# Kernel tuning notes

Measured on AMD Instinct MI355X. Metric: run time of the kernel, lower is better.

The kernel has to match this reference:

```python
import jax, jax.numpy as jnp
import numpy as np

B, N, DK, DM = 8, 4096, 512, 64

def setup_inputs() -> dict:
    key = jax.random.key(0)
    ks = jax.random.split(key, 7)
    K = jax.random.normal(ks[0], (B, N, DK), dtype=jnp.float32)
    Q = jax.random.normal(ks[1], (B, N, DK), dtype=jnp.float32)
    V = jax.random.normal(ks[2], (B, N, DK), dtype=jnp.float32)
    s = 1.0 / np.sqrt(DK)
    Wk = jax.random.normal(ks[3], (DM, DK), dtype=jnp.float32) * s
    bk = jax.random.normal(ks[4], (DM,), dtype=jnp.float32) * 0.01
    Wq = jax.random.normal(ks[5], (DM, DK), dtype=jnp.float32) * s
    bq = jax.random.normal(ks[6], (DM,), dtype=jnp.float32) * 0.01
    return {"K": K, "Q": Q, "V": V, "Wk": Wk, "bk": bk, "Wq": Wq, "bq": bq}

def reference(K, Q, V, Wk, bk, Wq, bq):
    # Linear projections (torch Linear: x @ W.T + b)
    pk = jnp.einsum('bnd,md->bnm', K, Wk) + bk  # [B,N,DM]
    pq = jnp.einsum('bnd,md->bnm', Q, Wq) + bq  # [B,M,DM]
    scale = 1.0 / np.sqrt(DM).astype(np.float32)
    scores = jnp.einsum('bqm,bkm->bqk', pq, pk) * scale  # [B,M,N]
    attn = jax.nn.softmax(scores, axis=-1)
    return jnp.einsum('bqk,bkd->bqd', attn, V)  # V unprojected, as in original
```

## Files before the change

kernel.cpp:

```cpp
#include <hip/hip_runtime.h>
#include <hip/hip_bf16.h>
#include <cstdint>


#define DEVINL __device__ __forceinline__

using f32x4  = __attribute__((ext_vector_type(4)))  float;
using bf16x8 = __attribute__((ext_vector_type(8)))  short;
using bf16x4 = __attribute__((ext_vector_type(4)))  short;

constexpr int BATCH = 8;
constexpr int N     = 4096;
constexpr int DK    = 512;
constexpr int DM    = 64;
constexpr int KVB   = 64;
constexpr int QB    = 128;
constexpr int STEPS = N / KVB;

DEVINL short cvt_bf16(float x) {
  uint32_t u = __float_as_uint(x);
  uint32_t r = u + 0x7fffu + ((u >> 16) & 1u);
  return (short)(r >> 16);
}

DEVINL void async16(void* lds, const void* g) {
  __builtin_amdgcn_global_load_lds(
      (const __attribute__((address_space(1))) uint32_t*)(uintptr_t)g,
      (__attribute__((address_space(3))) uint32_t*)(uint32_t)(uintptr_t)lds,
      16, 0, 0);
}

DEVINL f32x4 mfma16(bf16x8 a, bf16x8 b, f32x4 c) {
  return __builtin_amdgcn_mfma_f32_16x16x32_bf16(a, b, c, 0, 0, 0);
}

__global__ __launch_bounds__(256) void wconv_kernel(
    const float* __restrict__ Wk, const float* __restrict__ Wq,
    short* __restrict__ WkB, short* __restrict__ WqB) {
  int i = blockIdx.x * 256 + threadIdx.x;
  WkB[i] = cvt_bf16(Wk[i]);
  WqB[i] = cvt_bf16(Wq[i]);
}

__global__ __launch_bounds__(256) void vtrans_kernel(
    const float* __restrict__ V, short* __restrict__ Vt) {
  int bb = blockIdx.x;
  int b  = bb >> 9;
  int nt = (bb >> 3) & 63;
  int dt = bb & 7;
  int n0 = nt * 64, d0 = dt * 64;
  __shared__ short t_lds[64][80];
  int tid = threadIdx.x;
#pragma unroll
  for (int it = 0; it < 4; ++it) {
    int idx = it * 256 + tid;
    int row = idx >> 4;
    int c4  = idx & 15;
    f32x4 v = *(const f32x4*)&V[((size_t)b * N + n0 + row) * DK + d0 + c4 * 4];
#pragma unroll
    for (int j = 0; j < 4; ++j) t_lds[c4 * 4 + j][row] = cvt_bf16(v[j]);
  }
  __syncthreads();
#pragma unroll
  for (int it = 0; it < 2; ++it) {
    int idx = it * 256 + tid;
    int rd = idx >> 3;
    int ck = idx & 7;
    bf16x8 vv = *(const bf16x8*)&t_lds[rd][ck * 8];
    *(bf16x8*)&Vt[((size_t)b * DK + d0 + rd) * N + n0 + ck * 8] = vv;
  }
}

__global__ __launch_bounds__(512, 2) void proj_kernel(
    const float* __restrict__ Q, const float* __restrict__ K,
    const short* __restrict__ WqB, const short* __restrict__ WkB,
    const float* __restrict__ bq, const float* __restrict__ bk,
    short* __restrict__ pq, short* __restrict__ pk) {
  bool isK = blockIdx.x >= 256;
  const float* X    = isK ? K : Q;
  const short* W    = isK ? WkB : WqB;
  const float* bias = isK ? bk : bq;
  short* P          = isK ? pk : pq;
  int rb = (blockIdx.x & 255) * 128;

  __shared__ short x_lds[128 * 512];
  int tid = threadIdx.x, w = tid >> 6, lane = tid & 63, g = lane >> 4, c = lane & 15;

#pragma unroll
  for (int it = 0; it < 32; ++it) {
    int idx4 = it * 512 + tid;
    int row  = idx4 >> 7;
    int col  = (idx4 & 127) * 4;
    f32x4 v = *(const f32x4*)&X[((size_t)rb + row) * DK + col];
    bf16x4 hb;
#pragma unroll
    for (int j = 0; j < 4; ++j) hb[j] = cvt_bf16(v[j]);
    int sc = (col >> 3) ^ (row & 7);
    *(bf16x4*)&x_lds[row * 512 + sc * 8 + ((col >> 2) & 1) * 4] = hb;
  }
  __syncthreads();

  f32x4 o[4];
#pragma unroll
  for (int mt = 0; mt < 4; ++mt) o[mt] = f32x4{0.f, 0.f, 0.f, 0.f};
  int arow = w * 16 + c;
#pragma unroll
  for (int ks = 0; ks < 16; ++ks) {
    int sc = (ks * 4 + g) ^ (arow & 7);
    bf16x8 a = *(const bf16x8*)&x_lds[arow * 512 + sc * 8];
#pragma unroll
    for (int mt = 0; mt < 4; ++mt) {
      bf16x8 bfr = *(const bf16x8*)&W[(size_t)(mt * 16 + c) * DK + ks * 32 + g * 8];
      o[mt] = mfma16(a, bfr, o[mt]);
    }
  }
#pragma unroll
  for (int mt = 0; mt < 4; ++mt) {
    float bb = bias[mt * 16 + c];
#pragma unroll
    for (int r = 0; r < 4; ++r) {
      int row = rb + w * 16 + g * 4 + r;
      P[(size_t)row * DM + mt * 16 + c] = cvt_bf16(o[mt][r] + bb);
    }
  }
}

__global__ __launch_bounds__(512, 2) void flash_kernel(
    const short* __restrict__ pq, const short* __restrict__ pk,
    const short* __restrict__ vt, float* __restrict__ out) {
  int b  = blockIdx.x & 7;
  int qt = blockIdx.x >> 3;
  int q0 = qt * QB;

  int tid = threadIdx.x, w = tid >> 6, lane = tid & 63, g = lane >> 4, c = lane & 15;

  __shared__ short pk_lds[KVB * DM];
  __shared__ short vt_lds[2][DK * KVB];
  __shared__ short p_lds[QB * KVB];
  __shared__ float alpha_lds[QB];
  __shared__ float lsum_lds[QB];

  const short* pk_b = pk + (size_t)b * N * DM;
  const short* vt_b = vt + (size_t)b * DK * N;

  const short* pq_row = pq + ((size_t)b * N + q0 + w * 16 + c) * DM;
  bf16x8 qf0 = *(const bf16x8*)(pq_row + g * 8);
  bf16x8 qf1 = *(const bf16x8*)(pq_row + 32 + g * 8);

  f32x4 acc[4][8];
#pragma unroll
  for (int i = 0; i < 4; ++i)
#pragma unroll
    for (int j = 0; j < 8; ++j) acc[i][j] = f32x4{0.f, 0.f, 0.f, 0.f};

  float m_run = -1e30f, l_run = 0.f;

  auto stage_pk = [&](int t) {
    int off16 = tid;
    int row = off16 >> 3, ck = off16 & 7;
    const short* src = pk_b + (size_t)(t * KVB + row) * DM + ((ck ^ (row & 7)) * 8);
    async16((void*)(pk_lds + (size_t)w * 512), (const void*)src);
  };
  auto stage_vt = [&](int t, int buf) {
#pragma unroll
    for (int r = 0; r < 8; ++r) {
      int off16 = r * 512 + tid;
      int row = off16 >> 3, ck = off16 & 7;
      const short* src = vt_b + (size_t)row * N + t * KVB + ((ck ^ (row & 7)) * 8);
      async16((void*)(&vt_lds[buf][0] + (size_t)(r * 512 + w * 64) * 8), (const void*)src);
    }
  };

  stage_pk(0);
  stage_vt(0, 0);
  __syncthreads();

  for (int t = 0; t < STEPS; ++t) {
    int buf = t & 1;
    if (t + 1 < STEPS) stage_vt(t + 1, buf ^ 1);

    float sv[16];
#pragma unroll
    for (int s = 0; s < 4; ++s) {
      int row = s * 16 + c;
      bf16x8 a0 = *(const bf16x8*)&pk_lds[row * 64 + ((g ^ (row & 7)) * 8)];
      bf16x8 a1 = *(const bf16x8*)&pk_lds[row * 64 + (((4 + g) ^ (row & 7)) * 8)];
      f32x4 d = f32x4{0.f, 0.f, 0.f, 0.f};
      d = mfma16(a0, qf0, d);
      d = mfma16(a1, qf1, d);
#pragma unroll
      for (int r = 0; r < 4; ++r) sv[s * 4 + r] = d[r] * 0.125f;
    }

    float tmax = sv[0];
#pragma unroll
    for (int j = 1; j < 16; ++j) tmax = fmaxf(tmax, sv[j]);
    tmax = fmaxf(tmax, __shfl_xor(tmax, 16));
    tmax = fmaxf(tmax, __shfl_xor(tmax, 32));
    float m_new = fmaxf(m_run, tmax);
    float alpha = __expf(m_run - m_new);
    float ts = 0.f;
#pragma unroll
    for (int j = 0; j < 16; ++j) { sv[j] = __expf(sv[j] - m_new); ts += sv[j]; }
    ts += __shfl_xor(ts, 16);
    ts += __shfl_xor(ts, 32);
    l_run = l_run * alpha + ts;
    m_run = m_new;

    int qrow = w * 16 + c;
    if (g == 0) alpha_lds[qrow] = alpha;
#pragma unroll
    for (int s = 0; s < 4; ++s) {
      bf16x4 pb;
#pragma unroll
      for (int r = 0; r < 4; ++r) pb[r] = cvt_bf16(sv[s * 4 + r]);
      int ck = (s * 2 + (g >> 1)) ^ (qrow & 7);
      *(bf16x4*)&p_lds[qrow * 64 + ck * 8 + (g & 1) * 4] = pb;
    }

    asm volatile("s_waitcnt lgkmcnt(0)" ::: "memory");
    __builtin_amdgcn_s_barrier();
    asm volatile("" ::: "memory");

    if (t + 1 < STEPS) stage_pk(t + 1);

    float al[8];
#pragma unroll
    for (int j = 0; j < 8; ++j) al[j] = alpha_lds[j * 16 + c];
#pragma unroll
    for (int i = 0; i < 4; ++i)
#pragma unroll
      for (int j = 0; j < 8; ++j) acc[i][j] *= al[j];

#pragma unroll
    for (int kh = 0; kh < 2; ++kh) {
      bf16x8 pf[8];
#pragma unroll
      for (int j = 0; j < 8; ++j) {
        int row = j * 16 + c;
        pf[j] = *(const bf16x8*)&p_lds[row * 64 + (((kh * 4 + g) ^ (row & 7)) * 8)];
      }
#pragma unroll
      for (int i = 0; i < 4; ++i) {
        int row = w * 64 + i * 16 + c;
        bf16x8 vf = *(const bf16x8*)&vt_lds[buf][row * 64 + (((kh * 4 + g) ^ (row & 7)) * 8)];
#pragma unroll
        for (int j = 0; j < 8; ++j) acc[i][j] = mfma16(vf, pf[j], acc[i][j]);
      }
    }
    __syncthreads();
  }

  if (g == 0) lsum_lds[w * 16 + c] = l_run;
  __syncthreads();

  float* out_b = out + (size_t)b * N * DK;
#pragma unroll
  for (int j = 0; j < 8; ++j) {
    float rl = 1.f / lsum_lds[j * 16 + c];
#pragma unroll
    for (int i = 0; i < 4; ++i)
#pragma unroll
      for (int r = 0; r < 4; ++r) {
        int q    = q0 + j * 16 + c;
        int vcol = w * 64 + i * 16 + g * 4 + r;
        out_b[(size_t)q * DK + vcol] = acc[i][j][r] * rl;
      }
  }
}

extern "C" void kernel_launch(void* const* d_in, const int* in_sizes, int n_in,
                              void* d_out, int out_size, void* d_ws, size_t ws_size,
                              hipStream_t stream) {
  (void)in_sizes; (void)n_in; (void)out_size; (void)ws_size;
  const float* K  = (const float*)d_in[0];
  const float* Q  = (const float*)d_in[1];
  const float* V  = (const float*)d_in[2];
  const float* Wk = (const float*)d_in[3];
  const float* bk = (const float*)d_in[4];
  const float* Wq = (const float*)d_in[5];
  const float* bq = (const float*)d_in[6];
  float* out = (float*)d_out;

  char* ws = (char*)d_ws;
  short* pq  = (short*)(ws + 0);
  short* pk  = (short*)(ws + ((size_t)4 << 20));
  short* vt  = (short*)(ws + ((size_t)8 << 20));
  short* WqB = (short*)(ws + ((size_t)40 << 20));
  short* WkB = (short*)(ws + ((size_t)40 << 20) + 64 * 512 * 2);

  hipLaunchKernelGGL(wconv_kernel,  dim3(128),  dim3(256), 0, stream, Wk, Wq, WkB, WqB);
  hipLaunchKernelGGL(vtrans_kernel, dim3(4096), dim3(256), 0, stream, V, vt);
  hipLaunchKernelGGL(proj_kernel,   dim3(512),  dim3(512), 0, stream, Q, K, WqB, WkB, bq, bk, pq, pk);
  hipLaunchKernelGGL(flash_kernel,  dim3(256),  dim3(512), 0, stream, pq, pk, vt, out);
}
```

Before: 267.5 us.

## Software-pipeline flash loop: overlap next QK softmax with PV MFMAs, lazy rescale

```diff
diff --git a/kernel.cpp b/kernel.cpp
--- a/kernel.cpp
+++ b/kernel.cpp
@@ -81,6 +81,7 @@
   const short* W    = isK ? WkB : WqB;
   const float* bias = isK ? bk : bq;
   short* P          = isK ? pk : pq;
+  float sc          = isK ? 1.0f : 0.125f;
   int rb = (blockIdx.x & 255) * 128;
 
   __shared__ short x_lds[128 * 512];
@@ -95,8 +96,8 @@
     bf16x4 hb;
 #pragma unroll
     for (int j = 0; j < 4; ++j) hb[j] = cvt_bf16(v[j]);
-    int sc = (col >> 3) ^ (row & 7);
-    *(bf16x4*)&x_lds[row * 512 + sc * 8 + ((col >> 2) & 1) * 4] = hb;
+    int scz = (col >> 3) ^ (row & 7);
+    *(bf16x4*)&x_lds[row * 512 + scz * 8 + ((col >> 2) & 1) * 4] = hb;
   }
   __syncthreads();
 
@@ -106,8 +107,8 @@
   int arow = w * 16 + c;
 #pragma unroll
   for (int ks = 0; ks < 16; ++ks) {
-    int sc = (ks * 4 + g) ^ (arow & 7);
-    bf16x8 a = *(const bf16x8*)&x_lds[arow * 512 + sc * 8];
+    int scz = (ks * 4 + g) ^ (arow & 7);
+    bf16x8 a = *(const bf16x8*)&x_lds[arow * 512 + scz * 8];
 #pragma unroll
     for (int mt = 0; mt < 4; ++mt) {
       bf16x8 bfr = *(const bf16x8*)&W[(size_t)(mt * 16 + c) * DK + ks * 32 + g * 8];
@@ -120,7 +121,7 @@
 #pragma unroll
     for (int r = 0; r < 4; ++r) {
       int row = rb + w * 16 + g * 4 + r;
-      P[(size_t)row * DM + mt * 16 + c] = cvt_bf16(o[mt][r] + bb);
+      P[(size_t)row * DM + mt * 16 + c] = cvt_bf16((o[mt][r] + bb) * sc);
     }
   }
 }
@@ -133,6 +134,7 @@
   int q0 = qt * QB;
 
   int tid = threadIdx.x, w = tid >> 6, lane = tid & 63, g = lane >> 4, c = lane & 15;
+  int qrow = w * 16 + c;
 
   __shared__ short pk_lds[KVB * DM];
   __shared__ short vt_lds[2][DK * KVB];
@@ -143,7 +145,7 @@
   const short* pk_b = pk + (size_t)b * N * DM;
   const short* vt_b = vt + (size_t)b * DK * N;
 
-  const short* pq_row = pq + ((size_t)b * N + q0 + w * 16 + c) * DM;
+  const short* pq_row = pq + ((size_t)b * N + q0 + qrow) * DM;
   bf16x8 qf0 = *(const bf16x8*)(pq_row + g * 8);
   bf16x8 qf1 = *(const bf16x8*)(pq_row + 32 + g * 8);
 
@@ -156,8 +158,7 @@
   float m_run = -1e30f, l_run = 0.f;
 
   auto stage_pk = [&](int t) {
-    int off16 = tid;
-    int row = off16 >> 3, ck = off16 & 7;
+    int row = tid >> 3, ck = tid & 7;
     const short* src = pk_b + (size_t)(t * KVB + row) * DM + ((ck ^ (row & 7)) * 8);
     async16((void*)(pk_lds + (size_t)w * 512), (const void*)src);
   };
@@ -175,11 +176,10 @@
   stage_vt(0, 0);
   __syncthreads();
 
-  for (int t = 0; t < STEPS; ++t) {
-    int buf = t & 1;
-    if (t + 1 < STEPS) stage_vt(t + 1, buf ^ 1);
-
-    float sv[16];
+  float sv[16];
+  bf16x4 pb[4];
+  float alpha;
+  {
 #pragma unroll
     for (int s = 0; s < 4; ++s) {
       int row = s * 16 + c;
@@ -189,49 +189,161 @@
       d = mfma16(a0, qf0, d);
       d = mfma16(a1, qf1, d);
 #pragma unroll
-      for (int r = 0; r < 4; ++r) sv[s * 4 + r] = d[r] * 0.125f;
-    }
-
+      for (int r = 0; r < 4; ++r) sv[s * 4 + r] = d[r];
+    }
     float tmax = sv[0];
 #pragma unroll
     for (int j = 1; j < 16; ++j) tmax = fmaxf(tmax, sv[j]);
     tmax = fmaxf(tmax, __shfl_xor(tmax, 16));
     tmax = fmaxf(tmax, __shfl_xor(tmax, 32));
-    float m_new = fmaxf(m_run, tmax);
-    float alpha = __expf(m_run - m_new);
+    m_run = tmax;
     float ts = 0.f;
 #pragma unroll
-    for (int j = 0; j < 16; ++j) { sv[j] = __expf(sv[j] - m_new); ts += sv[j]; }
+    for (int j = 0; j < 16; ++j) { sv[j] = __expf(sv[j] - m_run); ts += sv[j]; }
+    ts += __shfl_xor(ts, 16);
+    ts += __shfl_xor(ts, 32);
+    l_run = ts;
+    alpha = 1.0f;
+#pragma unroll
+    for (int s = 0; s < 4; ++s)
+#pragma unroll
+      for (int r = 0; r < 4; ++r) pb[s][r] = cvt_bf16(sv[s * 4 + r]);
+  }
+  asm volatile("s_waitcnt lgkmcnt(0)" ::: "memory");
+  __builtin_amdgcn_s_barrier();
+#pragma unroll
+  for (int s = 0; s < 4; ++s) {
+    int ck = (s * 2 + (g >> 1)) ^ (qrow & 7);
+    *(bf16x4*)&p_lds[qrow * 64 + ck * 8 + (g & 1) * 4] = pb[s];
+  }
+  if (g == 0) alpha_lds[qrow] = alpha;
+  stage_pk(1);
+  asm volatile("s_waitcnt lgkmcnt(0)" ::: "memory");
+  __builtin_amdgcn_s_barrier();
+  __builtin_amdgcn_sched_barrier(0);
+
+  for (int t = 0; t < STEPS - 1; ++t) {
+    int vb = t & 1;
+    stage_vt(t + 1, vb ^ 1);
+    asm volatile("s_waitcnt vmcnt(8)" ::: "memory");
+    __builtin_amdgcn_sched_barrier(0);
+
+    {
+      float al[8];
+      bool ne = false;
+#pragma unroll
+      for (int j = 0; j < 8; ++j) { al[j] = alpha_lds[j * 16 + c]; ne |= (al[j] != 1.0f); }
+      if (__any(ne)) {
+#pragma unroll
+        for (int i = 0; i < 4; ++i)
+#pragma unroll
+          for (int j = 0; j < 8; ++j) acc[i][j] *= al[j];
+      }
+    }
+
+#pragma unroll
+    for (int s = 0; s < 4; ++s) {
+      int row = s * 16 + c;
+      bf16x8 a0 = *(const bf16x8*)&pk_lds[row * 64 + ((g ^ (row & 7)) * 8)];
+      bf16x8 a1 = *(const bf16x8*)&pk_lds[row * 64 + (((4 + g) ^ (row & 7)) * 8)];
+      f32x4 d = f32x4{0.f, 0.f, 0.f, 0.f};
+      d = mfma16(a0, qf0, d);
+      d = mfma16(a1, qf1, d);
+#pragma unroll
+      for (int r = 0; r < 4; ++r) sv[s * 4 + r] = d[r];
+    }
+
+    float tmax = sv[0];
+#pragma unroll
+    for (int j = 1; j < 16; ++j) tmax = fmaxf(tmax, sv[j]);
+    tmax = fmaxf(tmax, __shfl_xor(tmax, 16));
+    tmax = fmaxf(tmax, __shfl_xor(tmax, 32));
+    alpha = 1.0f;
+    if (tmax > m_run + 8.0f) {
+      alpha = __expf(m_run - tmax);
+      m_run = tmax;
+    }
+
+    __builtin_amdgcn_s_setprio(1);
+    {
+      bf16x8 pf[8];
+#pragma unroll
+      for (int j = 0; j < 8; ++j) {
+        int row = j * 16 + c;
+        pf[j] = *(const bf16x8*)&p_lds[row * 64 + ((g ^ (row & 7)) * 8)];
+      }
+#pragma unroll
+      for (int i = 0; i < 4; ++i) {
+        int row = w * 64 + i * 16 + c;
+        bf16x8 vf = *(const bf16x8*)&vt_lds[vb][row * 64 + ((g ^ (row & 7)) * 8)];
+#pragma unroll
+        for (int j = 0; j < 8; ++j) acc[i][j] = mfma16(vf, pf[j], acc[i][j]);
+      }
+    }
+    __builtin_amdgcn_s_setprio(0);
+
+    float ts = 0.f;
+#pragma unroll
+    for (int j = 0; j < 16; ++j) { sv[j] = __expf(sv[j] - m_run); ts += sv[j]; }
+
+    __builtin_amdgcn_s_setprio(1);
+    {
+      bf16x8 pf[8];
+#pragma unroll
+      for (int j = 0; j < 8; ++j) {
+        int row = j * 16 + c;
+        pf[j] = *(const bf16x8*)&p_lds[row * 64 + (((4 + g) ^ (row & 7)) * 8)];
+      }
+#pragma unroll
+      for (int i = 0; i < 4; ++i) {
+        int row = w * 64 + i * 16 + c;
+        bf16x8 vf = *(const bf16x8*)&vt_lds[vb][row * 64 + (((4 + g) ^ (row & 7)) * 8)];
+#pragma unroll
+        for (int j = 0; j < 8; ++j) acc[i][j] = mfma16(vf, pf[j], acc[i][j]);
+      }
+    }
+    __builtin_amdgcn_s_setprio(0);
+
     ts += __shfl_xor(ts, 16);
     ts += __shfl_xor(ts, 32);
     l_run = l_run * alpha + ts;
-    m_run = m_new;
-
-    int qrow = w * 16 + c;
-    if (g == 0) alpha_lds[qrow] = alpha;
-#pragma unroll
-    for (int s = 0; s < 4; ++s) {
-      bf16x4 pb;
-#pragma unroll
-      for (int r = 0; r < 4; ++r) pb[r] = cvt_bf16(sv[s * 4 + r]);
-      int ck = (s * 2 + (g >> 1)) ^ (qrow & 7);
-      *(bf16x4*)&p_lds[qrow * 64 + ck * 8 + (g & 1) * 4] = pb;
-    }
+#pragma unroll
+    for (int s = 0; s < 4; ++s)
+#pragma unroll
+      for (int r = 0; r < 4; ++r) pb[s][r] = cvt_bf16(sv[s * 4 + r]);
 
     asm volatile("s_waitcnt lgkmcnt(0)" ::: "memory");
     __builtin_amdgcn_s_barrier();
-    asm volatile("" ::: "memory");
-
-    if (t + 1 < STEPS) stage_pk(t + 1);
-
+    __builtin_amdgcn_sched_barrier(0);
+
+#pragma unroll
+    for (int s = 0; s < 4; ++s) {
+      int ck = (s * 2 + (g >> 1)) ^ (qrow & 7);
+      *(bf16x4*)&p_lds[qrow * 64 + ck * 8 + (g & 1) * 4] = pb[s];
+    }
+    if (g == 0) alpha_lds[qrow] = alpha;
+    if (t < STEPS - 2) stage_pk(t + 2);
+    asm volatile("s_waitcnt lgkmcnt(0)" ::: "memory");
+    __builtin_amdgcn_s_barrier();
+    __builtin_amdgcn_sched_barrier(0);
+  }
+
+  asm volatile("s_waitcnt vmcnt(0)" ::: "memory");
+  __builtin_amdgcn_sched_barrier(0);
+  {
     float al[8];
-#pragma unroll
-    for (int j = 0; j < 8; ++j) al[j] = alpha_lds[j * 16 + c];
-#pragma unroll
-    for (int i = 0; i < 4; ++i)
-#pragma unroll
-      for (int j = 0; j < 8; ++j) acc[i][j] *= al[j];
-
+    bool ne = false;
+#pragma unroll
+    for (int j = 0; j < 8; ++j) { al[j] = alpha_lds[j * 16 + c]; ne |= (al[j] != 1.0f); }
+    if (__any(ne)) {
+#pragma unroll
+      for (int i = 0; i < 4; ++i)
+#pragma unroll
+        for (int j = 0; j < 8; ++j) acc[i][j] *= al[j];
+    }
+  }
+  {
+    int vb = (STEPS - 1) & 1;
 #pragma unroll
     for (int kh = 0; kh < 2; ++kh) {
       bf16x8 pf[8];
@@ -243,16 +355,16 @@
 #pragma unroll
       for (int i = 0; i < 4; ++i) {
         int row = w * 64 + i * 16 + c;
-        bf16x8 vf = *(const bf16x8*)&vt_lds[buf][row * 64 + (((kh * 4 + g) ^ (row & 7)) * 8)];
+        bf16x8 vf = *(const bf16x8*)&vt_lds[vb][row * 64 + (((kh * 4 + g) ^ (row & 7)) * 8)];
 #pragma unroll
         for (int j = 0; j < 8; ++j) acc[i][j] = mfma16(vf, pf[j], acc[i][j]);
       }
     }
-    __syncthreads();
-  }
-
-  if (g == 0) lsum_lds[w * 16 + c] = l_run;
-  __syncthreads();
+  }
+
+  if (g == 0) lsum_lds[qrow] = l_run;
+  asm volatile("s_waitcnt lgkmcnt(0)" ::: "memory");
+  __builtin_amdgcn_s_barrier();
 
   float* out_b = out + (size_t)b * N * DK;
 #pragma unroll
```

Result: faster. 248.7 us (-7.0%).

## Restructure flash kernel with register-streamed K/V and lazy softmax rescaling

Applied to the files above, without the earlier changes.

```diff
diff --git a/kernel.cpp b/kernel.cpp
--- a/kernel.cpp
+++ b/kernel.cpp
@@ -13,9 +13,12 @@
 constexpr int N     = 4096;
 constexpr int DK    = 512;
 constexpr int DM    = 64;
-constexpr int KVB   = 64;
-constexpr int QB    = 128;
+constexpr int KVB   = 32;
+constexpr int QB    = 64;
 constexpr int STEPS = N / KVB;
+
+#define PQ_SCALE 0.18033688011112042f
+#define DEFER_THR 11.5f
 
 DEVINL short cvt_bf16(float x) {
   uint32_t u = __float_as_uint(x);
@@ -23,16 +26,20 @@
   return (short)(r >> 16);
 }
 
-DEVINL void async16(void* lds, const void* g) {
-  __builtin_amdgcn_global_load_lds(
-      (const __attribute__((address_space(1))) uint32_t*)(uintptr_t)g,
-      (__attribute__((address_space(3))) uint32_t*)(uint32_t)(uintptr_t)lds,
-      16, 0, 0);
+DEVINL uint32_t cvtpk(float lo, float hi) {
+  uint32_t r;
+  asm("v_cvt_pk_bf16_f32 %0, %1, %2" : "=v"(r) : "v"(lo), "v"(hi));
+  return r;
 }
 
 DEVINL f32x4 mfma16(bf16x8 a, bf16x8 b, f32x4 c) {
   return __builtin_amdgcn_mfma_f32_16x16x32_bf16(a, b, c, 0, 0, 0);
 }
+
+#define LGKM0_BAR() do { \
+  asm volatile("s_waitcnt lgkmcnt(0)" ::: "memory"); \
+  __builtin_amdgcn_s_barrier(); \
+} while (0)
 
 __global__ __launch_bounds__(256) void wconv_kernel(
     const float* __restrict__ Wk, const float* __restrict__ Wq,
@@ -81,6 +88,7 @@
   const short* W    = isK ? WkB : WqB;
   const float* bias = isK ? bk : bq;
   short* P          = isK ? pk : pq;
+  float sc          = isK ? 1.0f : PQ_SCALE;
   int rb = (blockIdx.x & 255) * 128;
 
   __shared__ short x_lds[128 * 512];
@@ -95,8 +103,8 @@
     bf16x4 hb;
 #pragma unroll
     for (int j = 0; j < 4; ++j) hb[j] = cvt_bf16(v[j]);
-    int sc = (col >> 3) ^ (row & 7);
-    *(bf16x4*)&x_lds[row * 512 + sc * 8 + ((col >> 2) & 1) * 4] = hb;
+    int scz = (col >> 3) ^ (row & 7);
+    *(bf16x4*)&x_lds[row * 512 + scz * 8 + ((col >> 2) & 1) * 4] = hb;
   }
   __syncthreads();
 
@@ -106,8 +114,8 @@
   int arow = w * 16 + c;
 #pragma unroll
   for (int ks = 0; ks < 16; ++ks) {
-    int sc = (ks * 4 + g) ^ (arow & 7);
-    bf16x8 a = *(const bf16x8*)&x_lds[arow * 512 + sc * 8];
+    int scz = (ks * 4 + g) ^ (arow & 7);
+    bf16x8 a = *(const bf16x8*)&x_lds[arow * 512 + scz * 8];
 #pragma unroll
     for (int mt = 0; mt < 4; ++mt) {
       bf16x8 bfr = *(const bf16x8*)&W[(size_t)(mt * 16 + c) * DK + ks * 32 + g * 8];
@@ -120,12 +128,12 @@
 #pragma unroll
     for (int r = 0; r < 4; ++r) {
       int row = rb + w * 16 + g * 4 + r;
-      P[(size_t)row * DM + mt * 16 + c] = cvt_bf16(o[mt][r] + bb);
-    }
-  }
-}
-
-__global__ __launch_bounds__(512, 2) void flash_kernel(
+      P[(size_t)row * DM + mt * 16 + c] = cvt_bf16((o[mt][r] + bb) * sc);
+    }
+  }
+}
+
+__global__ __launch_bounds__(512, 4) void flash_kernel(
     const short* __restrict__ pq, const short* __restrict__ pk,
     const short* __restrict__ vt, float* __restrict__ out) {
   int b  = blockIdx.x & 7;
@@ -133,139 +141,180 @@
   int q0 = qt * QB;
 
   int tid = threadIdx.x, w = tid >> 6, lane = tid & 63, g = lane >> 4, c = lane & 15;
-
-  __shared__ short pk_lds[KVB * DM];
-  __shared__ short vt_lds[2][DK * KVB];
-  __shared__ short p_lds[QB * KVB];
+  int qg = w & 3, kh = w >> 2;
+  int qrow = qg * 16 + c;
+
+  __shared__ short p_lds[QB * 40];
+  __shared__ float partmax[2][QB];
   __shared__ float alpha_lds[QB];
-  __shared__ float lsum_lds[QB];
-
-  const short* pk_b = pk + (size_t)b * N * DM;
-  const short* vt_b = vt + (size_t)b * DK * N;
-
-  const short* pq_row = pq + ((size_t)b * N + q0 + w * 16 + c) * DM;
+  __shared__ float lsum2[2][QB];
+  __shared__ unsigned long long aflag8;
+
+  const short* pfr = p_lds + c * 40 + g * 8;
+  short*       pw  = p_lds + qrow * 40 + kh * 16 + g * 4;
+
+  const short* a_src = pk + (size_t)b * N * DM + (size_t)(kh * 16 + c) * DM + g * 8;
+  const short* v_src = vt + (size_t)b * DK * N + (size_t)(w * 64 + c) * N + g * 8;
+
+  const short* pq_row = pq + ((size_t)b * N + q0 + qrow) * DM;
   bf16x8 qf0 = *(const bf16x8*)(pq_row + g * 8);
   bf16x8 qf1 = *(const bf16x8*)(pq_row + 32 + g * 8);
 
-  f32x4 acc[4][8];
+  f32x4 acc[4][4];
 #pragma unroll
   for (int i = 0; i < 4; ++i)
 #pragma unroll
-    for (int j = 0; j < 8; ++j) acc[i][j] = f32x4{0.f, 0.f, 0.f, 0.f};
-
-  float m_run = -1e30f, l_run = 0.f;
-
-  auto stage_pk = [&](int t) {
-    int off16 = tid;
-    int row = off16 >> 3, ck = off16 & 7;
-    const short* src = pk_b + (size_t)(t * KVB + row) * DM + ((ck ^ (row & 7)) * 8);
-    async16((void*)(pk_lds + (size_t)w * 512), (const void*)src);
-  };
-  auto stage_vt = [&](int t, int buf) {
-#pragma unroll
-    for (int r = 0; r < 8; ++r) {
-      int off16 = r * 512 + tid;
-      int row = off16 >> 3, ck = off16 & 7;
-      const short* src = vt_b + (size_t)row * N + t * KVB + ((ck ^ (row & 7)) * 8);
-      async16((void*)(&vt_lds[buf][0] + (size_t)(r * 512 + w * 64) * 8), (const void*)src);
-    }
-  };
-
-  stage_pk(0);
-  stage_vt(0, 0);
-  __syncthreads();
-
-  for (int t = 0; t < STEPS; ++t) {
-    int buf = t & 1;
-    if (t + 1 < STEPS) stage_vt(t + 1, buf ^ 1);
-
-    float sv[16];
-#pragma unroll
-    for (int s = 0; s < 4; ++s) {
-      int row = s * 16 + c;
-      bf16x8 a0 = *(const bf16x8*)&pk_lds[row * 64 + ((g ^ (row & 7)) * 8)];
-      bf16x8 a1 = *(const bf16x8*)&pk_lds[row * 64 + (((4 + g) ^ (row & 7)) * 8)];
-      f32x4 d = f32x4{0.f, 0.f, 0.f, 0.f};
-      d = mfma16(a0, qf0, d);
-      d = mfma16(a1, qf1, d);
-#pragma unroll
-      for (int r = 0; r < 4; ++r) sv[s * 4 + r] = d[r] * 0.125f;
-    }
-
-    float tmax = sv[0];
-#pragma unroll
-    for (int j = 1; j < 16; ++j) tmax = fmaxf(tmax, sv[j]);
+    for (int j = 0; j < 4; ++j) acc[i][j] = f32x4{0.f, 0.f, 0.f, 0.f};
+
+  float m_run, l_run;
+  f32x4 sv;
+  uint32_t pb0, pb1;
+  float alpha;
+
+  bf16x8 An0 = *(const bf16x8*)(a_src);
+  bf16x8 An1 = *(const bf16x8*)(a_src + 32);
+  a_src += KVB * DM;
+  bf16x8 VF0 = *(const bf16x8*)(v_src);
+  bf16x8 VF1 = *(const bf16x8*)(v_src + 16 * N);
+  bf16x8 VF2 = *(const bf16x8*)(v_src + 32 * N);
+  bf16x8 VF3 = *(const bf16x8*)(v_src + 48 * N);
+  __builtin_amdgcn_sched_barrier(0);
+
+  {
+    f32x4 d = f32x4{0.f, 0.f, 0.f, 0.f};
+    d = mfma16(An0, qf0, d);
+    d = mfma16(An1, qf1, d);
+    sv = d;
+    float tmax = fmaxf(fmaxf(sv[0], sv[1]), fmaxf(sv[2], sv[3]));
     tmax = fmaxf(tmax, __shfl_xor(tmax, 16));
     tmax = fmaxf(tmax, __shfl_xor(tmax, 32));
-    float m_new = fmaxf(m_run, tmax);
-    float alpha = __expf(m_run - m_new);
+    if (g == 0) partmax[kh][qrow] = tmax;
+    LGKM0_BAR();
+    float om = partmax[1 ^ kh][qrow];
+    m_run = fmaxf(tmax, om);
     float ts = 0.f;
 #pragma unroll
-    for (int j = 0; j < 16; ++j) { sv[j] = __expf(sv[j] - m_new); ts += sv[j]; }
+    for (int r = 0; r < 4; ++r) { sv[r] = exp2f(sv[r] - m_run); ts += sv[r]; }
+    ts += __shfl_xor(ts, 16);
+    ts += __shfl_xor(ts, 32);
+    l_run = ts;
+    pb0 = cvtpk(sv[0], sv[1]);
+    pb1 = cvtpk(sv[2], sv[3]);
+  }
+  An0 = *(const bf16x8*)(a_src);
+  An1 = *(const bf16x8*)(a_src + 32);
+  a_src += KVB * DM;
+  *(uint2*)pw = uint2{pb0, pb1};
+  if (kh == 0 && g == 0) alpha_lds[qrow] = 1.0f;
+  if (lane == 0) ((unsigned char*)&aflag8)[w] = 0;
+  LGKM0_BAR();
+
+  for (int t = 0; t < STEPS - 1; ++t) {
+    v_src += KVB;
+    bf16x8 VN0 = *(const bf16x8*)(v_src);
+    bf16x8 VN1 = *(const bf16x8*)(v_src + 16 * N);
+    bf16x8 VN2 = *(const bf16x8*)(v_src + 32 * N);
+    bf16x8 VN3 = *(const bf16x8*)(v_src + 48 * N);
+    __builtin_amdgcn_sched_barrier(0);
+
+    f32x4 d = f32x4{0.f, 0.f, 0.f, 0.f};
+    d = mfma16(An0, qf0, d);
+    d = mfma16(An1, qf1, d);
+    sv = d;
+    float tmax = fmaxf(fmaxf(sv[0], sv[1]), fmaxf(sv[2], sv[3]));
+    tmax = fmaxf(tmax, __shfl_xor(tmax, 16));
+    tmax = fmaxf(tmax, __shfl_xor(tmax, 32));
+    if (g == 0) partmax[kh][qrow] = tmax;
+    LGKM0_BAR();
+
+    float om = partmax[1 ^ kh][qrow];
+    unsigned long long flg = aflag8;
+    float tm = fmaxf(tmax, om);
+    alpha = 1.0f;
+    if (tm > m_run + DEFER_THR) {
+      alpha = exp2f(m_run - tm);
+      m_run = tm;
+    }
+    float ts = 0.f;
+#pragma unroll
+    for (int r = 0; r < 4; ++r) { sv[r] = exp2f(sv[r] - m_run); ts += sv[r]; }
     ts += __shfl_xor(ts, 16);
     ts += __shfl_xor(ts, 32);
     l_run = l_run * alpha + ts;
-    m_run = m_new;
-
-    int qrow = w * 16 + c;
-    if (g == 0) alpha_lds[qrow] = alpha;
-#pragma unroll
-    for (int s = 0; s < 4; ++s) {
-      bf16x4 pb;
-#pragma unroll
-      for (int r = 0; r < 4; ++r) pb[r] = cvt_bf16(sv[s * 4 + r]);
-      int ck = (s * 2 + (g >> 1)) ^ (qrow & 7);
-      *(bf16x4*)&p_lds[qrow * 64 + ck * 8 + (g & 1) * 4] = pb;
-    }
-
-    asm volatile("s_waitcnt lgkmcnt(0)" ::: "memory");
-    __builtin_amdgcn_s_barrier();
-    asm volatile("" ::: "memory");
-
-    if (t + 1 < STEPS) stage_pk(t + 1);
-
-    float al[8];
-#pragma unroll
-    for (int j = 0; j < 8; ++j) al[j] = alpha_lds[j * 16 + c];
-#pragma unroll
-    for (int i = 0; i < 4; ++i)
-#pragma unroll
-      for (int j = 0; j < 8; ++j) acc[i][j] *= al[j];
-
-#pragma unroll
-    for (int kh = 0; kh < 2; ++kh) {
-      bf16x8 pf[8];
-#pragma unroll
-      for (int j = 0; j < 8; ++j) {
-        int row = j * 16 + c;
-        pf[j] = *(const bf16x8*)&p_lds[row * 64 + (((kh * 4 + g) ^ (row & 7)) * 8)];
+    pb0 = cvtpk(sv[0], sv[1]);
+    pb1 = cvtpk(sv[2], sv[3]);
+
+    if (flg) {
+#pragma unroll
+      for (int j = 0; j < 4; ++j) {
+        float al = alpha_lds[j * 16 + c];
+#pragma unroll
+        for (int i = 0; i < 4; ++i) acc[i][j] *= al;
       }
-#pragma unroll
-      for (int i = 0; i < 4; ++i) {
-        int row = w * 64 + i * 16 + c;
-        bf16x8 vf = *(const bf16x8*)&vt_lds[buf][row * 64 + (((kh * 4 + g) ^ (row & 7)) * 8)];
-#pragma unroll
-        for (int j = 0; j < 8; ++j) acc[i][j] = mfma16(vf, pf[j], acc[i][j]);
+    }
+
+    __builtin_amdgcn_s_setprio(1);
+#pragma unroll
+    for (int j = 0; j < 4; ++j) {
+      bf16x8 pf = *(const bf16x8*)(pfr + j * 640);
+      acc[0][j] = mfma16(VF0, pf, acc[0][j]);
+      acc[1][j] = mfma16(VF1, pf, acc[1][j]);
+      acc[2][j] = mfma16(VF2, pf, acc[2][j]);
+      acc[3][j] = mfma16(VF3, pf, acc[3][j]);
+    }
+    __builtin_amdgcn_s_setprio(0);
+
+    if (t < STEPS - 2) {
+      An0 = *(const bf16x8*)(a_src);
+      An1 = *(const bf16x8*)(a_src + 32);
+      a_src += KVB * DM;
+    }
+    LGKM0_BAR();
+
+    *(uint2*)pw = uint2{pb0, pb1};
+    if (kh == 0 && g == 0) alpha_lds[qrow] = alpha;
+    {
+      int any = __any(alpha != 1.0f);
+      if (lane == 0) ((unsigned char*)&aflag8)[w] = (unsigned char)any;
+    }
+    VF0 = VN0; VF1 = VN1; VF2 = VN2; VF3 = VN3;
+  }
+
+  LGKM0_BAR();
+  {
+    unsigned long long flg = aflag8;
+    if (flg) {
+#pragma unroll
+      for (int j = 0; j < 4; ++j) {
+        float al = alpha_lds[j * 16 + c];
+#pragma unroll
+        for (int i = 0; i < 4; ++i) acc[i][j] *= al;
       }
     }
-    __syncthreads();
-  }
-
-  if (g == 0) lsum_lds[w * 16 + c] = l_run;
-  __syncthreads();
+#pragma unroll
+    for (int j = 0; j < 4; ++j) {
+      bf16x8 pf = *(const bf16x8*)(pfr + j * 640);
+      acc[0][j] = mfma16(VF0, pf, acc[0][j]);
+      acc[1][j] = mfma16(VF1, pf, acc[1][j]);
+      acc[2][j] = mfma16(VF2, pf, acc[2][j]);
+      acc[3][j] = mfma16(VF3, pf, acc[3][j]);
+    }
+  }
+
+  if (g == 0) lsum2[kh][qrow] = l_run;
+  LGKM0_BAR();
 
   float* out_b = out + (size_t)b * N * DK;
 #pragma unroll
-  for (int j = 0; j < 8; ++j) {
-    float rl = 1.f / lsum_lds[j * 16 + c];
-#pragma unroll
-    for (int i = 0; i < 4; ++i)
-#pragma unroll
-      for (int r = 0; r < 4; ++r) {
-        int q    = q0 + j * 16 + c;
-        int vcol = w * 64 + i * 16 + g * 4 + r;
-        out_b[(size_t)q * DK + vcol] = acc[i][j][r] * rl;
-      }
+  for (int j = 0; j < 4; ++j) {
+    int q = q0 + j * 16 + c;
+    float rl = 1.f / (lsum2[0][j * 16 + c] + lsum2[1][j * 16 + c]);
+#pragma unroll
+    for (int i = 0; i < 4; ++i) {
+      f32x4 o = acc[i][j];
+      o[0] *= rl; o[1] *= rl; o[2] *= rl; o[3] *= rl;
+      *(f32x4*)&out_b[(size_t)q * DK + w * 64 + i * 16 + g * 4] = o;
+    }
   }
 }
 
@@ -292,5 +341,5 @@
   hipLaunchKernelGGL(wconv_kernel,  dim3(128),  dim3(256), 0, stream, Wk, Wq, WkB, WqB);
   hipLaunchKernelGGL(vtrans_kernel, dim3(4096), dim3(256), 0, stream, V, vt);
   hipLaunchKernelGGL(proj_kernel,   dim3(512),  dim3(512), 0, stream, Q, K, WqB, WkB, bq, bk, pq, pk);
-  hipLaunchKernelGGL(flash_kernel,  dim3(256),  dim3(512), 0, stream, pq, pk, vt, out);
-}
+  hipLaunchKernelGGL(flash_kernel,  dim3(512),  dim3(512), 0, stream, pq, pk, vt, out);
+}
```

Measured after the change: 648.7 us. 143% more time.
